# Kernel tuning notes

Measured on AMD Instinct MI355X. Metric: run time of the kernel, lower is better.

Reference implementation:

```python
import jax, jax.numpy as jnp
import numpy as np

NB_LAYERS, KSIZE = 4, 5
DILATIONS = [1, 2, 4, 8]
NEG_SLOPE = 0.1
BN_EPS = 1e-5


def _cont_conv(times, feats, mask, dilation, p):
    """One ContConv1d layer: causal gather of time-diffs -> kernel MLP -> weighted aggregate + skip + BN."""
    k1W, k1b, k2W, k2b, k3W, k3b, skipW, skipb, gamma, beta = p
    bs, L, Cin = feats.shape
    Cout = skipW.shape[1]
    lags = jnp.arange(KSIZE) * dilation                    # (K,) include_zero_lag=True -> lag 0 included
    idx = jnp.arange(L)[None, :] - lags[:, None]           # (K, L) causal neighbor indices
    valid = idx >= 0
    idx_c = jnp.clip(idx, 0, L - 1)
    g_times = times[:, idx_c]                              # (bs, K, L)
    g_feats = feats[:, idx_c, :]                           # (bs, K, L, Cin)
    g_mask = (mask[:, idx_c] & valid[None] & mask[:, None, :]).astype(feats.dtype)
    dt = (times[:, None, :] - g_times) * g_mask            # (bs, K, L) zeroed where invalid
    # kernel MLP: scalar time-diff -> (Cin, Cout) mixing matrix
    h = jax.nn.leaky_relu(dt[..., None] @ k1W + k1b, NEG_SLOPE)
    h = jax.nn.leaky_relu(h @ k2W + k2b, NEG_SLOPE)
    kv = (h @ k3W + k3b).reshape(bs, KSIZE, L, Cin, Cout) * g_mask[..., None, None]
    out = jnp.einsum('bklc,bklcd->bld', g_feats, kv)       # aggregate over taps and input channels
    out = out + feats @ skipW + skipb                      # 1x1-conv skip connection
    mu = out.mean((0, 1))                                  # BatchNorm1d (training-mode batch stats)
    var = out.var((0, 1))
    return (out - mu) * jax.lax.rsqrt(var + BN_EPS) * gamma + beta


def _ccnn_forward(event_times, event_types, emb, k1W, k1b, k2W, k2b, k3W, k3b, skipW, skipb, gamma, beta):
    bs = event_times.shape[0]
    emb = emb.at[0].set(0.0)                               # padding_idx = 0
    times = jnp.concatenate([jnp.zeros((bs, 1), event_times.dtype), event_times], axis=1)
    bos = jnp.full((bs, 1), jnp.max(event_types) + 1, dtype=event_types.dtype)
    types = jnp.concatenate([bos, event_types], axis=1)
    mask = times != 0                                      # BOS (t=0) masked, as in the original
    enc = emb[types]                                       # (bs, L+1, C)
    for i in range(NB_LAYERS):
        p = (k1W[i], k1b[i], k2W[i], k2b[i], k3W[i], k3b[i], skipW[i], skipb[i], gamma[i], beta[i])
        enc = jax.nn.leaky_relu(_cont_conv(times, enc, mask, DILATIONS[i], p), NEG_SLOPE)
    return enc


def setup_inputs() -> dict:
    key = jax.random.key(0)
    ks = jax.random.split(key, 12)
    bs, L, C, H, num_types = 8, 2048, 32, 16, 100
    s = 0.05
    gaps = jax.random.uniform(ks[0], (bs, L)) * 0.1 + 0.01
    times = jnp.cumsum(gaps, axis=1)                       # strictly increasing positive event times
    types = jax.random.randint(ks[1], (bs, L), 0, num_types) + 1   # 1..num_types
    pad = jnp.arange(L) >= int(0.9 * L)
    times = jnp.where(pad[None, :], 0.0, times).astype(jnp.float32)
    types = jnp.where(pad[None, :], 0, types).astype(jnp.int32)
    return {
        'event_times': times,
        'event_types': types,
        'emb': jax.random.normal(ks[2], (num_types + 2, C)) * s,
        'k1W': jax.random.normal(ks[3], (NB_LAYERS, 1, H)) * s,
        'k1b': jnp.zeros((NB_LAYERS, H)),
        'k2W': jax.random.normal(ks[4], (NB_LAYERS, H, H)) * s,
        'k2b': jnp.zeros((NB_LAYERS, H)),
        'k3W': jax.random.normal(ks[5], (NB_LAYERS, H, C * C)) * s,
        'k3b': jnp.zeros((NB_LAYERS, C * C)),
        'skipW': jax.random.normal(ks[6], (NB_LAYERS, C, C)) * s,
        'skipb': jnp.zeros((NB_LAYERS, C)),
        'gamma': jnp.ones((NB_LAYERS, C)),
        'beta': jnp.zeros((NB_LAYERS, C)),
    }


def reference(event_times, event_types, emb, k1W, k1b, k2W, k2b, k3W, k3b, skipW, skipb, gamma, beta):
    return _ccnn_forward(event_times, event_types, emb, k1W, k1b, k2W, k2b, k3W, k3b, skipW, skipb, gamma, beta)
```

## Files before the change

### kernel.cpp

```cpp
#include <hip/hip_runtime.h>
#include <stdint.h>

#define NB_LAYERS 4
#define KSIZE 5
#define BSZ 8
#define LIN 2048
#define LSEQ 2049
#define CCH 32
#define HCH 16
#define MROWS (BSZ*LSEQ)
#define NTILES ((MROWS+15)/16)
#define KDIM 576
#define NEG 0.1f
#define BNEPS 1e-5f

typedef _Float16 h2v __attribute__((ext_vector_type(2)));
typedef _Float16 h8v __attribute__((ext_vector_type(8)));
typedef float    f4v __attribute__((ext_vector_type(4)));

union H8 { h8v v; h2v h[4]; };

static __device__ __forceinline__ h2v mkh2(float a, float b) {
  h2v r; r[0] = (_Float16)a; r[1] = (_Float16)b; return r;
}

__global__ void init_kernel(float* stats, int* maxp) {
  int i = blockIdx.x * blockDim.x + threadIdx.x;
  if (i < NB_LAYERS * 64) stats[i] = 0.f;
  if (i == 0) *maxp = 0;
}

__global__ void max_kernel(const int* __restrict__ types, int* maxp) {
  int i = blockIdx.x * blockDim.x + threadIdx.x;
  int v = 0;
  if (i < BSZ * LIN) v = types[i];
#pragma unroll
  for (int off = 32; off; off >>= 1) v = max(v, __shfl_xor(v, off, 64));
  if ((threadIdx.x & 63) == 0) atomicMax(maxp, v);
}

__global__ void prep_kernel(const float* __restrict__ k3W, const float* __restrict__ k3b,
                            const float* __restrict__ skipW, _Float16* __restrict__ Wt) {
  int id = blockIdx.x * blockDim.x + threadIdx.x;
  if (id >= NB_LAYERS * CCH * KDIM) return;
  int layer = id / (CCH * KDIM);
  int rem = id % (CCH * KDIM);
  int n = rem / KDIM;
  int k = rem % KDIM;
  float val;
  if (k < 512)      { int h = k >> 5, c = k & 31; val = k3W[layer*16384 + h*1024 + c*32 + n]; }
  else if (k < 544) { int c = k - 512;            val = k3b[layer*1024 + c*32 + n]; }
  else              { int c = k - 544;            val = skipW[layer*1024 + c*32 + n]; }
  Wt[id] = (_Float16)val;
}

__global__ void embed_kernel(const int* __restrict__ types, const float* __restrict__ emb,
                             const int* __restrict__ maxp, float* __restrict__ enc) {
  int id = blockIdx.x * blockDim.x + threadIdx.x;
  if (id >= MROWS * CCH) return;
  int row = id >> 5, c = id & 31;
  int b = row / LSEQ, pos = row % LSEQ;
  int t = (pos == 0) ? (*maxp + 1) : types[b * LIN + pos - 1];
  enc[id] = (t == 0) ? 0.f : emb[t * CCH + c];
}

__global__ __launch_bounds__(256) void conv_kernel(
    const float* __restrict__ enc_in, float* __restrict__ enc_out,
    const float* __restrict__ etimes,
    const float* __restrict__ k1Wp, const float* __restrict__ k1bp,
    const float* __restrict__ k2Wp, const float* __restrict__ k2bp,
    const _Float16* __restrict__ Wt,
    float* __restrict__ stats, int dil)
{
  __shared__ float sst[64];
  if (threadIdx.x < 64) sst[threadIdx.x] = 0.f;
  __syncthreads();

  const int lane = threadIdx.x & 63;
  const int wv   = threadIdx.x >> 6;
  const int m    = lane & 15;
  const int q    = lane >> 4;

  float k1w[HCH], k1b[HCH], k2b[HCH];
#pragma unroll
  for (int h = 0; h < HCH; h++) { k1w[h] = k1Wp[h]; k1b[h] = k1bp[h]; k2b[h] = k2bp[h]; }

  const _Float16* wb0 = Wt + m * KDIM + q * 8;
  const _Float16* wb1 = Wt + (m + 16) * KDIM + q * 8;

  for (int tile = blockIdx.x * 4 + wv; tile < NTILES; tile += gridDim.x * 4) {
    int row = tile * 16 + m;
    bool rvalid = row < MROWS;
    int rowc = min(row, MROWS - 1);
    int b = rowc / LSEQ, pos = rowc % LSEQ;
    float t_l = (pos == 0) ? 0.f : etimes[b * LIN + pos - 1];
    bool mask_l = rvalid && (t_l != 0.f);

    h2v wh[KSIZE][8];
    h2v fh[KSIZE][4];
    h2v fself[4];
    float Fb[8];
#pragma unroll
    for (int jj = 0; jj < 8; jj++) Fb[jj] = 0.f;

#pragma unroll
    for (int tap = 0; tap < KSIZE; tap++) {
      int j = pos - tap * dil;
      int jc = max(j, 0);
      float t_j = (jc == 0) ? 0.f : etimes[b * LIN + jc - 1];
      bool gm = mask_l && (j >= 0) && (t_j != 0.f);
      float dt = gm ? (t_l - t_j) : 0.f;

      const float* fp = enc_in + (b * LSEQ + jc) * CCH + q * 8;
      float4 fA = *(const float4*)(fp);
      float4 fB = *(const float4*)(fp + 4);
      float fv[8] = {fA.x, fA.y, fA.z, fA.w, fB.x, fB.y, fB.z, fB.w};

      if (tap == 0) {
        float rv = rvalid ? 1.f : 0.f;
#pragma unroll
        for (int p = 0; p < 4; p++) fself[p] = mkh2(fv[2*p] * rv, fv[2*p+1] * rv);
      }
      float g = gm ? 1.f : 0.f;
#pragma unroll
      for (int jj = 0; jj < 8; jj++) Fb[jj] += g * fv[jj];
#pragma unroll
      for (int p = 0; p < 4; p++) fh[tap][p] = mkh2(fv[2*p], fv[2*p+1]);

      if (__ballot(gm)) {
        float h1[HCH];
#pragma unroll
        for (int h = 0; h < HCH; h++) { float x = fmaf(dt, k1w[h], k1b[h]); h1[h] = fmaxf(x, NEG * x); }
        float h2[HCH];
#pragma unroll
        for (int h = 0; h < HCH; h++) h2[h] = k2b[h];
#pragma unroll
        for (int hp = 0; hp < HCH; hp++) {
          float hv = h1[hp];
#pragma unroll
          for (int h = 0; h < HCH; h++) h2[h] = fmaf(hv, k2Wp[hp * HCH + h], h2[h]);
        }
#pragma unroll
        for (int hh = 0; hh < 8; hh++) {
          float a = h2[2*hh];     a = fmaxf(a, NEG * a) * g;
          float c2 = h2[2*hh+1];  c2 = fmaxf(c2, NEG * c2) * g;
          wh[tap][hh] = mkh2(a, c2);
        }
      } else {
#pragma unroll
        for (int hh = 0; hh < 8; hh++) wh[tap][hh] = mkh2(0.f, 0.f);
      }
    }

    f4v acc0 = {0.f, 0.f, 0.f, 0.f};
    f4v acc1 = {0.f, 0.f, 0.f, 0.f};

#pragma unroll
    for (int ks = 0; ks < 16; ks++) {
      H8 bf0, bf1, af;
      bf0.v = *(const h8v*)(wb0 + ks * 32);
      bf1.v = *(const h8v*)(wb1 + ks * 32);
      h2v u0 = mkh2(0.f,0.f), u1 = mkh2(0.f,0.f), u2 = mkh2(0.f,0.f), u3 = mkh2(0.f,0.f);
#pragma unroll
      for (int tap = 0; tap < KSIZE; tap++) {
        _Float16 w = wh[tap][ks >> 1][ks & 1];
        h2v wd; wd[0] = w; wd[1] = w;
        u0 += wd * fh[tap][0];
        u1 += wd * fh[tap][1];
        u2 += wd * fh[tap][2];
        u3 += wd * fh[tap][3];
      }
      af.h[0] = u0; af.h[1] = u1; af.h[2] = u2; af.h[3] = u3;
      acc0 = __builtin_amdgcn_mfma_f32_16x16x32_f16(af.v, bf0.v, acc0, 0, 0, 0);
      acc1 = __builtin_amdgcn_mfma_f32_16x16x32_f16(af.v, bf1.v, acc1, 0, 0, 0);
    }
    {
      H8 bf0, bf1, af;
      bf0.v = *(const h8v*)(wb0 + 512);
      bf1.v = *(const h8v*)(wb1 + 512);
#pragma unroll
      for (int p = 0; p < 4; p++) af.h[p] = mkh2(Fb[2*p], Fb[2*p+1]);
      acc0 = __builtin_amdgcn_mfma_f32_16x16x32_f16(af.v, bf0.v, acc0, 0, 0, 0);
      acc1 = __builtin_amdgcn_mfma_f32_16x16x32_f16(af.v, bf1.v, acc1, 0, 0, 0);
    }
    {
      H8 bf0, bf1, af;
      bf0.v = *(const h8v*)(wb0 + 544);
      bf1.v = *(const h8v*)(wb1 + 544);
      af.h[0] = fself[0]; af.h[1] = fself[1]; af.h[2] = fself[2]; af.h[3] = fself[3];
      acc0 = __builtin_amdgcn_mfma_f32_16x16x32_f16(af.v, bf0.v, acc0, 0, 0, 0);
      acc1 = __builtin_amdgcn_mfma_f32_16x16x32_f16(af.v, bf1.v, acc1, 0, 0, 0);
    }

    float s0 = 0.f, s1 = 0.f, s2 = 0.f, s3 = 0.f;
#pragma unroll
    for (int r = 0; r < 4; r++) {
      float v0 = acc0[r], v1 = acc1[r];
      s0 += v0; s1 += v0 * v0; s2 += v1; s3 += v1 * v1;
      int rd = tile * 16 + q * 4 + r;
      if (rd < MROWS) {
        enc_out[rd * CCH + m] = v0;
        enc_out[rd * CCH + 16 + m] = v1;
      }
    }
    s0 += __shfl_xor(s0, 16, 64); s0 += __shfl_xor(s0, 32, 64);
    s1 += __shfl_xor(s1, 16, 64); s1 += __shfl_xor(s1, 32, 64);
    s2 += __shfl_xor(s2, 16, 64); s2 += __shfl_xor(s2, 32, 64);
    s3 += __shfl_xor(s3, 16, 64); s3 += __shfl_xor(s3, 32, 64);
    if (q == 0) {
      atomicAdd(&sst[m], s0);
      atomicAdd(&sst[32 + m], s1);
      atomicAdd(&sst[16 + m], s2);
      atomicAdd(&sst[48 + m], s3);
    }
  }
  __syncthreads();
  if (threadIdx.x < 64) atomicAdd(&stats[threadIdx.x], sst[threadIdx.x]);
}

__global__ void bn_kernel(const float* __restrict__ x, float* __restrict__ out,
                          const float* __restrict__ stats,
                          const float* __restrict__ gamma, const float* __restrict__ beta) {
  int id = blockIdx.x * blockDim.x + threadIdx.x;
  if (id >= MROWS * CCH) return;
  int c = id & 31;
  const float inv = 1.f / (float)MROWS;
  float mu = stats[c] * inv;
  float var = stats[32 + c] * inv - mu * mu;
  float sc = gamma[c] * rsqrtf(var + BNEPS);
  float v = (x[id] - mu) * sc + beta[c];
  out[id] = fmaxf(v, NEG * v);
}

extern "C" void kernel_launch(void* const* d_in, const int* in_sizes, int n_in,
                              void* d_out, int out_size, void* d_ws, size_t ws_size,
                              hipStream_t stream) {
  (void)in_sizes; (void)n_in; (void)out_size; (void)ws_size;
  const float* event_times = (const float*)d_in[0];
  const int*   event_types = (const int*)d_in[1];
  const float* emb   = (const float*)d_in[2];
  const float* k1W   = (const float*)d_in[3];
  const float* k1b   = (const float*)d_in[4];
  const float* k2W   = (const float*)d_in[5];
  const float* k2b   = (const float*)d_in[6];
  const float* k3W   = (const float*)d_in[7];
  const float* k3b   = (const float*)d_in[8];
  const float* skipW = (const float*)d_in[9];
  const float* gamma = (const float*)d_in[11];
  const float* beta  = (const float*)d_in[12];

  float* enc_a = (float*)d_ws;
  float* enc_b = enc_a + (size_t)MROWS * CCH;
  float* stats = enc_b + (size_t)MROWS * CCH;
  int*   maxp  = (int*)(stats + NB_LAYERS * 64);
  _Float16* Wt = (_Float16*)(((uintptr_t)(maxp + 1) + 255) & ~(uintptr_t)255);

  init_kernel<<<2, 256, 0, stream>>>(stats, maxp);
  max_kernel<<<(BSZ * LIN + 255) / 256, 256, 0, stream>>>(event_types, maxp);
  prep_kernel<<<(NB_LAYERS * CCH * KDIM + 255) / 256, 256, 0, stream>>>(k3W, k3b, skipW, Wt);
  embed_kernel<<<(MROWS * CCH + 255) / 256, 256, 0, stream>>>(event_types, emb, maxp, enc_a);

  const int dils[NB_LAYERS] = {1, 2, 4, 8};
  for (int i = 0; i < NB_LAYERS; i++) {
    conv_kernel<<<256, 256, 0, stream>>>(enc_a, enc_b, event_times,
        k1W + i * HCH, k1b + i * HCH, k2W + i * HCH * HCH, k2b + i * HCH,
        Wt + (size_t)i * CCH * KDIM, stats + i * 64, dils[i]);
    float* nout = (i == NB_LAYERS - 1) ? (float*)d_out : enc_a;
    bn_kernel<<<(MROWS * CCH + 255) / 256, 256, 0, stream>>>(
        enc_b, nout, stats + i * 64, gamma + i * CCH, beta + i * CCH);
  }
}
```

Baseline: 176.5 us.

## Fuse all stages into one persistent kernel with grid-wide barriers

Replaces the chain of init, max, prep, embed, four conv and four BN launches with a single persistent kernel of 256 blocks that synchronises through an atomic-counter grid barrier. The BatchNorm and leaky-ReLU of each layer are folded into the next layer's gather by applying a per-channel scale and shift to loaded features, so the separate BN pass over the activations is dropped for the first three layers. This removes launch gaps and one read/write of the activation buffer per layer. In exchange it adds spin-wait barriers, which rely on all 256 blocks being co-resident, and recomputes the affine transform on each of the five tap loads.

```diff
diff --git a/kernel.cpp b/kernel.cpp
--- a/kernel.cpp
+++ b/kernel.cpp
@@ -13,6 +13,8 @@
 #define KDIM 576
 #define NEG 0.1f
 #define BNEPS 1e-5f
+#define NBLK 256
+#define NTHR 256
 
 typedef _Float16 h2v __attribute__((ext_vector_type(2)));
 typedef _Float16 h8v __attribute__((ext_vector_type(8)));
@@ -24,212 +26,273 @@
   h2v r; r[0] = (_Float16)a; r[1] = (_Float16)b; return r;
 }
 
-__global__ void init_kernel(float* stats, int* maxp) {
-  int i = blockIdx.x * blockDim.x + threadIdx.x;
+static __device__ __forceinline__ void gsync(int* cnt, int target) {
+  __threadfence();
+  __syncthreads();
+  if (threadIdx.x == 0) {
+    __hip_atomic_fetch_add(cnt, 1, __ATOMIC_ACQ_REL, __HIP_MEMORY_SCOPE_AGENT);
+    while (__hip_atomic_load(cnt, __ATOMIC_RELAXED, __HIP_MEMORY_SCOPE_AGENT) < target) {}
+  }
+  __syncthreads();
+  __threadfence();
+}
+
+__global__ void init_kernel(float* stats, int* cnt) {
+  int i = threadIdx.x;
   if (i < NB_LAYERS * 64) stats[i] = 0.f;
-  if (i == 0) *maxp = 0;
-}
-
-__global__ void max_kernel(const int* __restrict__ types, int* maxp) {
-  int i = blockIdx.x * blockDim.x + threadIdx.x;
-  int v = 0;
-  if (i < BSZ * LIN) v = types[i];
-#pragma unroll
-  for (int off = 32; off; off >>= 1) v = max(v, __shfl_xor(v, off, 64));
-  if ((threadIdx.x & 63) == 0) atomicMax(maxp, v);
-}
-
-__global__ void prep_kernel(const float* __restrict__ k3W, const float* __restrict__ k3b,
-                            const float* __restrict__ skipW, _Float16* __restrict__ Wt) {
-  int id = blockIdx.x * blockDim.x + threadIdx.x;
-  if (id >= NB_LAYERS * CCH * KDIM) return;
-  int layer = id / (CCH * KDIM);
-  int rem = id % (CCH * KDIM);
-  int n = rem / KDIM;
-  int k = rem % KDIM;
-  float val;
-  if (k < 512)      { int h = k >> 5, c = k & 31; val = k3W[layer*16384 + h*1024 + c*32 + n]; }
-  else if (k < 544) { int c = k - 512;            val = k3b[layer*1024 + c*32 + n]; }
-  else              { int c = k - 544;            val = skipW[layer*1024 + c*32 + n]; }
-  Wt[id] = (_Float16)val;
-}
-
-__global__ void embed_kernel(const int* __restrict__ types, const float* __restrict__ emb,
-                             const int* __restrict__ maxp, float* __restrict__ enc) {
-  int id = blockIdx.x * blockDim.x + threadIdx.x;
-  if (id >= MROWS * CCH) return;
-  int row = id >> 5, c = id & 31;
-  int b = row / LSEQ, pos = row % LSEQ;
-  int t = (pos == 0) ? (*maxp + 1) : types[b * LIN + pos - 1];
-  enc[id] = (t == 0) ? 0.f : emb[t * CCH + c];
-}
-
-__global__ __launch_bounds__(256) void conv_kernel(
-    const float* __restrict__ enc_in, float* __restrict__ enc_out,
-    const float* __restrict__ etimes,
-    const float* __restrict__ k1Wp, const float* __restrict__ k1bp,
-    const float* __restrict__ k2Wp, const float* __restrict__ k2bp,
-    const _Float16* __restrict__ Wt,
-    float* __restrict__ stats, int dil)
+  if (i == 0) *cnt = 0;
+}
+
+__global__ __launch_bounds__(NTHR) void mega_kernel(
+    const float* __restrict__ etimes, const int* __restrict__ types,
+    const float* __restrict__ emb,
+    const float* __restrict__ k1W, const float* __restrict__ k1b,
+    const float* __restrict__ k2W, const float* __restrict__ k2b,
+    const float* __restrict__ k3W, const float* __restrict__ k3b,
+    const float* __restrict__ skipW,
+    const float* __restrict__ gamma, const float* __restrict__ beta,
+    float* __restrict__ enc_a, float* __restrict__ enc_b,
+    _Float16* __restrict__ Wt, float* __restrict__ stats, int* cnt,
+    float* __restrict__ out)
 {
+  const int tid  = threadIdx.x;
+  const int gtid = blockIdx.x * NTHR + tid;
   __shared__ float sst[64];
-  if (threadIdx.x < 64) sst[threadIdx.x] = 0.f;
-  __syncthreads();
-
-  const int lane = threadIdx.x & 63;
-  const int wv   = threadIdx.x >> 6;
+  __shared__ int sm4[4];
+
+  for (int id = gtid; id < NB_LAYERS * CCH * KDIM; id += NBLK * NTHR) {
+    int layer = id / (CCH * KDIM);
+    int rem = id % (CCH * KDIM);
+    int n = rem / KDIM;
+    int k = rem % KDIM;
+    float val;
+    if (k < 512)      { int h = k >> 5, c = k & 31; val = k3W[layer*16384 + h*1024 + c*32 + n]; }
+    else if (k < 544) { int c = k - 512;            val = k3b[layer*1024 + c*32 + n]; }
+    else              { int c = k - 544;            val = skipW[layer*1024 + c*32 + n]; }
+    Wt[id] = (_Float16)val;
+  }
+  for (int id = gtid; id < MROWS * CCH; id += NBLK * NTHR) {
+    int row = id >> 5, c = id & 31;
+    int b = row / LSEQ, pos = row - b * LSEQ;
+    if (pos != 0) {
+      int t = types[b * LIN + pos - 1];
+      enc_a[id] = (t == 0) ? 0.f : emb[t * CCH + c];
+    }
+  }
+  if (blockIdx.x == 0) {
+    int v = 0;
+    for (int i = tid; i < BSZ * LIN; i += NTHR) v = max(v, types[i]);
+#pragma unroll
+    for (int off = 32; off; off >>= 1) v = max(v, __shfl_xor(v, off, 64));
+    if ((tid & 63) == 0) sm4[tid >> 6] = v;
+    __syncthreads();
+    int mx = max(max(sm4[0], sm4[1]), max(sm4[2], sm4[3]));
+    int b = tid >> 5, c = tid & 31;
+    enc_a[(b * LSEQ) * CCH + c] = emb[(mx + 1) * CCH + c];
+  }
+
+  int bt = NBLK;
+  gsync(cnt, bt); bt += NBLK;
+
+  const int lane = tid & 63;
+  const int wv   = tid >> 6;
   const int m    = lane & 15;
   const int q    = lane >> 4;
-
-  float k1w[HCH], k1b[HCH], k2b[HCH];
-#pragma unroll
-  for (int h = 0; h < HCH; h++) { k1w[h] = k1Wp[h]; k1b[h] = k1bp[h]; k2b[h] = k2bp[h]; }
-
-  const _Float16* wb0 = Wt + m * KDIM + q * 8;
-  const _Float16* wb1 = Wt + (m + 16) * KDIM + q * 8;
-
-  for (int tile = blockIdx.x * 4 + wv; tile < NTILES; tile += gridDim.x * 4) {
-    int row = tile * 16 + m;
-    bool rvalid = row < MROWS;
-    int rowc = min(row, MROWS - 1);
-    int b = rowc / LSEQ, pos = rowc % LSEQ;
-    float t_l = (pos == 0) ? 0.f : etimes[b * LIN + pos - 1];
-    bool mask_l = rvalid && (t_l != 0.f);
-
-    h2v wh[KSIZE][8];
-    h2v fh[KSIZE][4];
-    h2v fself[4];
-    float Fb[8];
-#pragma unroll
-    for (int jj = 0; jj < 8; jj++) Fb[jj] = 0.f;
-
-#pragma unroll
-    for (int tap = 0; tap < KSIZE; tap++) {
-      int j = pos - tap * dil;
-      int jc = max(j, 0);
-      float t_j = (jc == 0) ? 0.f : etimes[b * LIN + jc - 1];
-      bool gm = mask_l && (j >= 0) && (t_j != 0.f);
-      float dt = gm ? (t_l - t_j) : 0.f;
-
-      const float* fp = enc_in + (b * LSEQ + jc) * CCH + q * 8;
-      float4 fA = *(const float4*)(fp);
-      float4 fB = *(const float4*)(fp + 4);
-      float fv[8] = {fA.x, fA.y, fA.z, fA.w, fB.x, fB.y, fB.z, fB.w};
-
-      if (tap == 0) {
-        float rv = rvalid ? 1.f : 0.f;
-#pragma unroll
-        for (int p = 0; p < 4; p++) fself[p] = mkh2(fv[2*p] * rv, fv[2*p+1] * rv);
-      }
-      float g = gm ? 1.f : 0.f;
-#pragma unroll
-      for (int jj = 0; jj < 8; jj++) Fb[jj] += g * fv[jj];
-#pragma unroll
-      for (int p = 0; p < 4; p++) fh[tap][p] = mkh2(fv[2*p], fv[2*p+1]);
-
-      if (__ballot(gm)) {
-        float h1[HCH];
-#pragma unroll
-        for (int h = 0; h < HCH; h++) { float x = fmaf(dt, k1w[h], k1b[h]); h1[h] = fmaxf(x, NEG * x); }
-        float h2[HCH];
-#pragma unroll
-        for (int h = 0; h < HCH; h++) h2[h] = k2b[h];
-#pragma unroll
-        for (int hp = 0; hp < HCH; hp++) {
-          float hv = h1[hp];
-#pragma unroll
-          for (int h = 0; h < HCH; h++) h2[h] = fmaf(hv, k2Wp[hp * HCH + h], h2[h]);
-        }
-#pragma unroll
-        for (int hh = 0; hh < 8; hh++) {
-          float a = h2[2*hh];     a = fmaxf(a, NEG * a) * g;
-          float c2 = h2[2*hh+1];  c2 = fmaxf(c2, NEG * c2) * g;
-          wh[tap][hh] = mkh2(a, c2);
-        }
-      } else {
-#pragma unroll
-        for (int hh = 0; hh < 8; hh++) wh[tap][hh] = mkh2(0.f, 0.f);
-      }
+  const int dils[NB_LAYERS] = {1, 2, 4, 8};
+
+#pragma unroll 1
+  for (int layer = 0; layer < NB_LAYERS; layer++) {
+    const float* enc_in  = (layer & 1) ? enc_b : enc_a;
+    float*       enc_out = (layer & 1) ? enc_a : enc_b;
+    const int dil = dils[layer];
+    const float* k1Wp = k1W + layer * HCH;
+    const float* k1bp = k1b + layer * HCH;
+    const float* k2Wp = k2W + layer * HCH * HCH;
+    const float* k2bp = k2b + layer * HCH;
+    const _Float16* Wtl = Wt + layer * CCH * KDIM;
+    float* st_out = stats + layer * 64;
+
+    float sc[8], sh[8], slope;
+    if (layer > 0) {
+      const float* stp = stats + (layer - 1) * 64;
+      const float inv = 1.f / (float)MROWS;
+      const float* gp = gamma + (layer - 1) * CCH;
+      const float* bp = beta + (layer - 1) * CCH;
+#pragma unroll
+      for (int p = 0; p < 8; p++) {
+        int c = q * 8 + p;
+        float mu = stp[c] * inv;
+        float var = stp[32 + c] * inv - mu * mu;
+        float s = gp[c] * rsqrtf(var + BNEPS);
+        sc[p] = s; sh[p] = bp[c] - mu * s;
+      }
+      slope = NEG;
+    } else {
+#pragma unroll
+      for (int p = 0; p < 8; p++) { sc[p] = 1.f; sh[p] = 0.f; }
+      slope = 1.f;
     }
 
-    f4v acc0 = {0.f, 0.f, 0.f, 0.f};
-    f4v acc1 = {0.f, 0.f, 0.f, 0.f};
-
-#pragma unroll
-    for (int ks = 0; ks < 16; ks++) {
-      H8 bf0, bf1, af;
-      bf0.v = *(const h8v*)(wb0 + ks * 32);
-      bf1.v = *(const h8v*)(wb1 + ks * 32);
-      h2v u0 = mkh2(0.f,0.f), u1 = mkh2(0.f,0.f), u2 = mkh2(0.f,0.f), u3 = mkh2(0.f,0.f);
+    float k1w[HCH], k1bb[HCH], k2bb[HCH];
+#pragma unroll
+    for (int h = 0; h < HCH; h++) { k1w[h] = k1Wp[h]; k1bb[h] = k1bp[h]; k2bb[h] = k2bp[h]; }
+
+    const _Float16* wb0 = Wtl + m * KDIM + q * 8;
+    const _Float16* wb1 = Wtl + (m + 16) * KDIM + q * 8;
+
+    __syncthreads();
+    if (tid < 64) sst[tid] = 0.f;
+    __syncthreads();
+
+    for (int tile = blockIdx.x * 4 + wv; tile < NTILES; tile += NBLK * 4) {
+      int row = tile * 16 + m;
+      bool rvalid = row < MROWS;
+      int rowc = min(row, MROWS - 1);
+      int b = rowc / LSEQ, pos = rowc % LSEQ;
+      float t_l = (pos == 0) ? 0.f : etimes[b * LIN + pos - 1];
+      bool mask_l = rvalid && (t_l != 0.f);
+
+      h2v wh[KSIZE][8];
+      h2v fh[KSIZE][4];
+      h2v fself[4];
+      float Fb[8];
+#pragma unroll
+      for (int jj = 0; jj < 8; jj++) Fb[jj] = 0.f;
+
 #pragma unroll
       for (int tap = 0; tap < KSIZE; tap++) {
-        _Float16 w = wh[tap][ks >> 1][ks & 1];
-        h2v wd; wd[0] = w; wd[1] = w;
-        u0 += wd * fh[tap][0];
-        u1 += wd * fh[tap][1];
-        u2 += wd * fh[tap][2];
-        u3 += wd * fh[tap][3];
-      }
-      af.h[0] = u0; af.h[1] = u1; af.h[2] = u2; af.h[3] = u3;
-      acc0 = __builtin_amdgcn_mfma_f32_16x16x32_f16(af.v, bf0.v, acc0, 0, 0, 0);
-      acc1 = __builtin_amdgcn_mfma_f32_16x16x32_f16(af.v, bf1.v, acc1, 0, 0, 0);
+        int j = pos - tap * dil;
+        int jc = max(j, 0);
+        float t_j = (jc == 0) ? 0.f : etimes[b * LIN + jc - 1];
+        bool gm = mask_l && (j >= 0) && (t_j != 0.f);
+        float dt = gm ? (t_l - t_j) : 0.f;
+
+        const float* fp = enc_in + (b * LSEQ + jc) * CCH + q * 8;
+        float4 fA = *(const float4*)(fp);
+        float4 fB = *(const float4*)(fp + 4);
+        float fv[8] = {fA.x, fA.y, fA.z, fA.w, fB.x, fB.y, fB.z, fB.w};
+#pragma unroll
+        for (int jj = 0; jj < 8; jj++) {
+          float x = fmaf(fv[jj], sc[jj], sh[jj]);
+          fv[jj] = fmaxf(x, slope * x);
+        }
+
+        if (tap == 0) {
+          float rv = rvalid ? 1.f : 0.f;
+#pragma unroll
+          for (int p = 0; p < 4; p++) fself[p] = mkh2(fv[2*p] * rv, fv[2*p+1] * rv);
+        }
+        float g = gm ? 1.f : 0.f;
+#pragma unroll
+        for (int jj = 0; jj < 8; jj++) Fb[jj] += g * fv[jj];
+#pragma unroll
+        for (int p = 0; p < 4; p++) fh[tap][p] = mkh2(fv[2*p], fv[2*p+1]);
+
+        if (__ballot(gm)) {
+          float h1[HCH];
+#pragma unroll
+          for (int h = 0; h < HCH; h++) { float x = fmaf(dt, k1w[h], k1bb[h]); h1[h] = fmaxf(x, NEG * x); }
+          float h2[HCH];
+#pragma unroll
+          for (int h = 0; h < HCH; h++) h2[h] = k2bb[h];
+#pragma unroll
+          for (int hp = 0; hp < HCH; hp++) {
+            float hv = h1[hp];
+#pragma unroll
+            for (int h = 0; h < HCH; h++) h2[h] = fmaf(hv, k2Wp[hp * HCH + h], h2[h]);
+          }
+#pragma unroll
+          for (int hh = 0; hh < 8; hh++) {
+            float a  = h2[2*hh];    a  = fmaxf(a,  NEG * a)  * g;
+            float c2 = h2[2*hh+1];  c2 = fmaxf(c2, NEG * c2) * g;
+            wh[tap][hh] = mkh2(a, c2);
+          }
+        } else {
+#pragma unroll
+          for (int hh = 0; hh < 8; hh++) wh[tap][hh] = mkh2(0.f, 0.f);
+        }
+      }
+
+      f4v acc0 = {0.f, 0.f, 0.f, 0.f};
+      f4v acc1 = {0.f, 0.f, 0.f, 0.f};
+
+#pragma unroll
+      for (int ks = 0; ks < 16; ks++) {
+        H8 bf0, bf1, af;
+        bf0.v = *(const h8v*)(wb0 + ks * 32);
+        bf1.v = *(const h8v*)(wb1 + ks * 32);
+        h2v u0 = mkh2(0.f,0.f), u1 = mkh2(0.f,0.f), u2 = mkh2(0.f,0.f), u3 = mkh2(0.f,0.f);
+#pragma unroll
+        for (int tap = 0; tap < KSIZE; tap++) {
+          _Float16 w = wh[tap][ks >> 1][ks & 1];
+          h2v wd; wd[0] = w; wd[1] = w;
+          u0 += wd * fh[tap][0];
+          u1 += wd * fh[tap][1];
+          u2 += wd * fh[tap][2];
+          u3 += wd * fh[tap][3];
+        }
+        af.h[0] = u0; af.h[1] = u1; af.h[2] = u2; af.h[3] = u3;
+        acc0 = __builtin_amdgcn_mfma_f32_16x16x32_f16(af.v, bf0.v, acc0, 0, 0, 0);
+        acc1 = __builtin_amdgcn_mfma_f32_16x16x32_f16(af.v, bf1.v, acc1, 0, 0, 0);
+      }
+      {
+        H8 bf0, bf1, af;
+        bf0.v = *(const h8v*)(wb0 + 512);
+        bf1.v = *(const h8v*)(wb1 + 512);
+#pragma unroll
+        for (int p = 0; p < 4; p++) af.h[p] = mkh2(Fb[2*p], Fb[2*p+1]);
+        acc0 = __builtin_amdgcn_mfma_f32_16x16x32_f16(af.v, bf0.v, acc0, 0, 0, 0);
+        acc1 = __builtin_amdgcn_mfma_f32_16x16x32_f16(af.v, bf1.v, acc1, 0, 0, 0);
+      }
+      {
+        H8 bf0, bf1, af;
+        bf0.v = *(const h8v*)(wb0 + 544);
+        bf1.v = *(const h8v*)(wb1 + 544);
+        af.h[0] = fself[0]; af.h[1] = fself[1]; af.h[2] = fself[2]; af.h[3] = fself[3];
+        acc0 = __builtin_amdgcn_mfma_f32_16x16x32_f16(af.v, bf0.v, acc0, 0, 0, 0);
+        acc1 = __builtin_amdgcn_mfma_f32_16x16x32_f16(af.v, bf1.v, acc1, 0, 0, 0);
+      }
+
+      float s0 = 0.f, s1 = 0.f, s2 = 0.f, s3 = 0.f;
+#pragma unroll
+      for (int r = 0; r < 4; r++) {
+        float v0 = acc0[r], v1 = acc1[r];
+        s0 += v0; s1 += v0 * v0; s2 += v1; s3 += v1 * v1;
+        int rd = tile * 16 + q * 4 + r;
+        if (rd < MROWS) {
+          enc_out[rd * CCH + m] = v0;
+          enc_out[rd * CCH + 16 + m] = v1;
+        }
+      }
+      s0 += __shfl_xor(s0, 16, 64); s0 += __shfl_xor(s0, 32, 64);
+      s1 += __shfl_xor(s1, 16, 64); s1 += __shfl_xor(s1, 32, 64);
+      s2 += __shfl_xor(s2, 16, 64); s2 += __shfl_xor(s2, 32, 64);
+      s3 += __shfl_xor(s3, 16, 64); s3 += __shfl_xor(s3, 32, 64);
+      if (q == 0) {
+        atomicAdd(&sst[m], s0);
+        atomicAdd(&sst[32 + m], s1);
+        atomicAdd(&sst[16 + m], s2);
+        atomicAdd(&sst[48 + m], s3);
+      }
     }
-    {
-      H8 bf0, bf1, af;
-      bf0.v = *(const h8v*)(wb0 + 512);
-      bf1.v = *(const h8v*)(wb1 + 512);
-#pragma unroll
-      for (int p = 0; p < 4; p++) af.h[p] = mkh2(Fb[2*p], Fb[2*p+1]);
-      acc0 = __builtin_amdgcn_mfma_f32_16x16x32_f16(af.v, bf0.v, acc0, 0, 0, 0);
-      acc1 = __builtin_amdgcn_mfma_f32_16x16x32_f16(af.v, bf1.v, acc1, 0, 0, 0);
+
+    __syncthreads();
+    if (tid < 64) atomicAdd(&st_out[tid], sst[tid]);
+    gsync(cnt, bt); bt += NBLK;
+  }
+
+  {
+    const float* stp = stats + 3 * 64;
+    const float inv = 1.f / (float)MROWS;
+    for (int id = gtid; id < MROWS * CCH; id += NBLK * NTHR) {
+      int c = id & 31;
+      float mu = stp[c] * inv;
+      float var = stp[32 + c] * inv - mu * mu;
+      float s = gamma[3 * CCH + c] * rsqrtf(var + BNEPS);
+      float v = (enc_a[id] - mu) * s + beta[3 * CCH + c];
+      out[id] = fmaxf(v, NEG * v);
     }
-    {
-      H8 bf0, bf1, af;
-      bf0.v = *(const h8v*)(wb0 + 544);
-      bf1.v = *(const h8v*)(wb1 + 544);
-      af.h[0] = fself[0]; af.h[1] = fself[1]; af.h[2] = fself[2]; af.h[3] = fself[3];
-      acc0 = __builtin_amdgcn_mfma_f32_16x16x32_f16(af.v, bf0.v, acc0, 0, 0, 0);
-      acc1 = __builtin_amdgcn_mfma_f32_16x16x32_f16(af.v, bf1.v, acc1, 0, 0, 0);
-    }
-
-    float s0 = 0.f, s1 = 0.f, s2 = 0.f, s3 = 0.f;
-#pragma unroll
-    for (int r = 0; r < 4; r++) {
-      float v0 = acc0[r], v1 = acc1[r];
-      s0 += v0; s1 += v0 * v0; s2 += v1; s3 += v1 * v1;
-      int rd = tile * 16 + q * 4 + r;
-      if (rd < MROWS) {
-        enc_out[rd * CCH + m] = v0;
-        enc_out[rd * CCH + 16 + m] = v1;
-      }
-    }
-    s0 += __shfl_xor(s0, 16, 64); s0 += __shfl_xor(s0, 32, 64);
-    s1 += __shfl_xor(s1, 16, 64); s1 += __shfl_xor(s1, 32, 64);
-    s2 += __shfl_xor(s2, 16, 64); s2 += __shfl_xor(s2, 32, 64);
-    s3 += __shfl_xor(s3, 16, 64); s3 += __shfl_xor(s3, 32, 64);
-    if (q == 0) {
-      atomicAdd(&sst[m], s0);
-      atomicAdd(&sst[32 + m], s1);
-      atomicAdd(&sst[16 + m], s2);
-      atomicAdd(&sst[48 + m], s3);
-    }
-  }
-  __syncthreads();
-  if (threadIdx.x < 64) atomicAdd(&stats[threadIdx.x], sst[threadIdx.x]);
-}
-
-__global__ void bn_kernel(const float* __restrict__ x, float* __restrict__ out,
-                          const float* __restrict__ stats,
-                          const float* __restrict__ gamma, const float* __restrict__ beta) {
-  int id = blockIdx.x * blockDim.x + threadIdx.x;
-  if (id >= MROWS * CCH) return;
-  int c = id & 31;
-  const float inv = 1.f / (float)MROWS;
-  float mu = stats[c] * inv;
-  float var = stats[32 + c] * inv - mu * mu;
-  float sc = gamma[c] * rsqrtf(var + BNEPS);
-  float v = (x[id] - mu) * sc + beta[c];
-  out[id] = fmaxf(v, NEG * v);
+  }
 }
 
 extern "C" void kernel_launch(void* const* d_in, const int* in_sizes, int n_in,
@@ -252,21 +315,11 @@
   float* enc_a = (float*)d_ws;
   float* enc_b = enc_a + (size_t)MROWS * CCH;
   float* stats = enc_b + (size_t)MROWS * CCH;
-  int*   maxp  = (int*)(stats + NB_LAYERS * 64);
-  _Float16* Wt = (_Float16*)(((uintptr_t)(maxp + 1) + 255) & ~(uintptr_t)255);
-
-  init_kernel<<<2, 256, 0, stream>>>(stats, maxp);
-  max_kernel<<<(BSZ * LIN + 255) / 256, 256, 0, stream>>>(event_types, maxp);
-  prep_kernel<<<(NB_LAYERS * CCH * KDIM + 255) / 256, 256, 0, stream>>>(k3W, k3b, skipW, Wt);
-  embed_kernel<<<(MROWS * CCH + 255) / 256, 256, 0, stream>>>(event_types, emb, maxp, enc_a);
-
-  const int dils[NB_LAYERS] = {1, 2, 4, 8};
-  for (int i = 0; i < NB_LAYERS; i++) {
-    conv_kernel<<<256, 256, 0, stream>>>(enc_a, enc_b, event_times,
-        k1W + i * HCH, k1b + i * HCH, k2W + i * HCH * HCH, k2b + i * HCH,
-        Wt + (size_t)i * CCH * KDIM, stats + i * 64, dils[i]);
-    float* nout = (i == NB_LAYERS - 1) ? (float*)d_out : enc_a;
-    bn_kernel<<<(MROWS * CCH + 255) / 256, 256, 0, stream>>>(
-        enc_b, nout, stats + i * 64, gamma + i * CCH, beta + i * CCH);
-  }
-}
+  int*   cnt   = (int*)(stats + NB_LAYERS * 64);
+  _Float16* Wt = (_Float16*)(((uintptr_t)(cnt + 1) + 255) & ~(uintptr_t)255);
+
+  init_kernel<<<1, 256, 0, stream>>>(stats, cnt);
+  mega_kernel<<<NBLK, NTHR, 0, stream>>>(event_times, event_types, emb,
+      k1W, k1b, k2W, k2b, k3W, k3b, skipW, gamma, beta,
+      enc_a, enc_b, Wt, stats, cnt, (float*)d_out);
+}
```

Result: slower. 361.8 us (+105.0%).
